# Optimization experiments

Measured on AMD Instinct MI355X. Metric: run time of the kernel, lower is better.

The kernel has to match this reference:

```python
import jax, jax.numpy as jnp
import numpy as np

CUTOFF = 5.0
B, A, N, G, F = 32, 256, 64, 50, 128


def _ssp(v):
    # shifted softplus used by SchNet filter network
    return jax.nn.softplus(v) - jnp.log(2.0).astype(v.dtype)


def setup_inputs() -> dict:
    key = jax.random.key(0)
    ks = jax.random.split(key, 8)
    x = jax.random.normal(ks[0], (B, A, F), dtype=jnp.float32)
    r_ij = jax.random.uniform(ks[1], (B, A, N), dtype=jnp.float32) * 4.5
    f_ij = jax.random.normal(ks[2], (B, A, N, G), dtype=jnp.float32)
    pairwise_mask = jnp.ones((B, A, N), dtype=jnp.float32)
    neighbors = jax.random.randint(ks[3], (B, A, N), 0, A, dtype=jnp.int64)
    in2f_w = jax.random.normal(ks[4], (F, F), dtype=jnp.float32) / np.sqrt(F)
    fw1 = jax.random.normal(ks[5], (G, F), dtype=jnp.float32) / np.sqrt(G)
    fb1 = jnp.zeros((F,), dtype=jnp.float32)
    fw2 = jax.random.normal(ks[6], (F, F), dtype=jnp.float32) / np.sqrt(F)
    fb2 = jnp.zeros((F,), dtype=jnp.float32)
    return {"x": x, "r_ij": r_ij, "f_ij": f_ij, "pairwise_mask": pairwise_mask,
            "neighbors": neighbors, "in2f_w": in2f_w, "fw1": fw1, "fb1": fb1,
            "fw2": fw2, "fb2": fb2}


def reference(x, r_ij, f_ij, pairwise_mask, neighbors, in2f_w, fw1, fb1, fw2, fb2):
    # filter network: Dense(G->F, shifted softplus) -> Dense(F->F, linear)
    W = _ssp(jnp.einsum('bang,gf->banf', f_ij, fw1) + fb1)
    W = jnp.einsum('banh,hf->banf', W, fw2) + fb2          # (B,A,N,F)
    # cosine cutoff
    C = 0.5 * (jnp.cos(r_ij * (jnp.pi / CUTOFF)) + 1.0)
    C = C * (r_ij < CUTOFF).astype(r_ij.dtype)
    W = W * C[..., None]
    # in2f dense (no bias)
    y = jnp.einsum('bai,if->baf', x, in2f_w)               # (B,A,F)
    # gather neighbor features along atom axis
    b_idx = jnp.arange(B)[:, None, None]
    y_nbh = y[b_idx, neighbors]                             # (B,A,N,F)
    # elementwise filter multiply + masked sum over neighbor axis
    out = jnp.sum(y_nbh * W * pairwise_mask[..., None], axis=2)  # (B,A,F)
    return out
```

## Files before the change

### kernel.cpp

```cpp
#include <hip/hip_runtime.h>
#include <hip/hip_bf16.h>
#include <math.h>

#define Bdim 32
#define Adim 256
#define Ndim 64
#define Gdim 50
#define Fdim 128

typedef __attribute__((ext_vector_type(8)))  short short8;
typedef __attribute__((ext_vector_type(16))) float floatx16;

__device__ __forceinline__ unsigned short f2bf_u(float x) {
    __hip_bfloat16 h = __float2bfloat16(x);
    return __builtin_bit_cast(unsigned short, h);
}
__device__ __forceinline__ unsigned pk2bf(float a, float b) {
    return (unsigned)f2bf_u(a) | ((unsigned)f2bf_u(b) << 16);
}
__device__ __forceinline__ float bf2f(unsigned short v) {
    return __builtin_bit_cast(float, ((unsigned)v) << 16);
}
__device__ __forceinline__ float sspf(float v) {
    float t = __expf(-fabsf(v));
    return fmaxf(v, 0.0f) + __logf(1.0f + t) - 0.69314718056f;
}
__device__ __forceinline__ short8 mk8(unsigned a, unsigned b, unsigned c, unsigned d) {
    union { unsigned u[4]; short8 s; } t;
    t.u[0] = a; t.u[1] = b; t.u[2] = c; t.u[3] = d;
    return t.s;
}

__global__ __launch_bounds__(256) void in2f_mfma2(const float* __restrict__ x,
                                                  const float* __restrict__ w,
                                                  unsigned short* __restrict__ y) {
    __shared__ short sWT[128 * 132];
    __shared__ short sX [128 * 132];
    const int tid = threadIdx.x;

#pragma unroll 4
    for (int k = 0; k < 32; ++k) {
        int idx = tid + k * 256;
        float2 v = *(const float2*)(w + 2 * idx);
        int i = idx >> 6;
        int f = (2 * idx) & 127;
        sWT[f * 132 + i]       = (short)f2bf_u(v.x);
        sWT[(f + 1) * 132 + i] = (short)f2bf_u(v.y);
    }
    const float* xb = x + (size_t)blockIdx.x * (128 * 128);
#pragma unroll 4
    for (int k = 0; k < 32; ++k) {
        int idx = tid + k * 256;
        float2 v = *(const float2*)(xb + 2 * idx);
        int row = idx >> 6;
        int i = (2 * idx) & 127;
        *(unsigned*)&sX[row * 132 + i] = pk2bf(v.x, v.y);
    }
    __syncthreads();

    const int wv = tid >> 6, lane = tid & 63, lm = lane & 31, lh = lane >> 5;
    floatx16 acc[4];
#pragma unroll
    for (int jt = 0; jt < 4; ++jt)
#pragma unroll
        for (int e = 0; e < 16; ++e) acc[jt][e] = 0.0f;

#pragma unroll
    for (int ks = 0; ks < 8; ++ks) {
        int g0 = ks * 16 + lh * 8;
        const short* ap = &sX[(wv * 32 + lm) * 132 + g0];
        uint2 a0 = *(const uint2*)ap;
        uint2 a1 = *(const uint2*)(ap + 4);
        short8 a = mk8(a0.x, a0.y, a1.x, a1.y);
#pragma unroll
        for (int jt = 0; jt < 4; ++jt) {
            const short* bp = &sWT[(jt * 32 + lm) * 132 + g0];
            uint2 b0 = *(const uint2*)bp;
            uint2 b1 = *(const uint2*)(bp + 4);
            acc[jt] = __builtin_amdgcn_mfma_f32_32x32x16_bf16(
                a, mk8(b0.x, b0.y, b1.x, b1.y), acc[jt], 0, 0, 0);
        }
    }
    const int rbase = blockIdx.x * 128 + wv * 32;
#pragma unroll
    for (int jt = 0; jt < 4; ++jt)
#pragma unroll
        for (int r = 0; r < 16; ++r) {
            int row = rbase + (r & 3) + 8 * (r >> 2) + 4 * lh;
            y[(size_t)row * 128 + jt * 32 + lm] = f2bf_u(acc[jt][r]);
        }
}

#define SF1 68
#define NSP 4096
#define GRID2 1536

struct FijRegs { float2 p[13]; };

__device__ __forceinline__ FijRegs load_fij(const float* __restrict__ f_ij,
                                            int sp, int row, int lh) {
    FijRegs F;
    const float* base = f_ij + (size_t)sp * (2 * Ndim * Gdim) + row * Gdim;
#pragma unroll
    for (int ks = 0; ks < 3; ++ks) {
        int g0 = 16 * ks + 8 * lh;
#pragma unroll
        for (int j = 0; j < 4; ++j)
            F.p[ks * 4 + j] = *(const float2*)(base + g0 + 2 * j);
    }
    F.p[12] = *(const float2*)(base + 48);
    return F;
}

__device__ __forceinline__ void cf_body(
    int sp, int par, const FijRegs& F, int nsp, FijRegs& Fn,
    const float* __restrict__ f_ij, const float* __restrict__ r_ij,
    const float* __restrict__ mask, const int* __restrict__ nbr,
    const unsigned short* __restrict__ ybf, float* __restrict__ out,
    float4 fb2v, const short* sFw1, const short* sFw2,
    float (*sRed)[2][128], int wv, int lm, int lh, int row)
{
    short8 bfr[4];
#pragma unroll
    for (int ks = 0; ks < 3; ++ks)
        bfr[ks] = mk8(pk2bf(F.p[ks*4+0].x, F.p[ks*4+0].y),
                      pk2bf(F.p[ks*4+1].x, F.p[ks*4+1].y),
                      pk2bf(F.p[ks*4+2].x, F.p[ks*4+2].y),
                      pk2bf(F.p[ks*4+3].x, F.p[ks*4+3].y));
    {
        unsigned u0 = lh ? 0u : pk2bf(F.p[12].x, F.p[12].y);
        unsigned u1 = lh ? 0u : 0x00003F80u;
        bfr[3] = mk8(u0, u1, 0u, 0u);
    }
    if (nsp >= 0) Fn = load_fij(f_ij, nsp, row, lh);

    unsigned A2[8][4];
#pragma unroll
    for (int ft = 0; ft < 4; ++ft) {
        floatx16 a1;
#pragma unroll
        for (int e = 0; e < 16; ++e) a1[e] = 0.0f;
#pragma unroll
        for (int ks = 0; ks < 4; ++ks) {
            const short* ap = &sFw1[(ft * 32 + lm) * SF1 + ks * 16 + lh * 8];
            uint2 a0 = *(const uint2*)ap;
            uint2 a1v = *(const uint2*)(ap + 4);
            a1 = __builtin_amdgcn_mfma_f32_32x32x16_bf16(
                mk8(a0.x, a0.y, a1v.x, a1v.y), bfr[ks], a1, 0, 0, 0);
        }
        unsigned P[8], X[8];
#pragma unroll
        for (int q = 0; q < 8; ++q)
            P[q] = pk2bf(sspf(a1[2 * q]), sspf(a1[2 * q + 1]));
#pragma unroll
        for (int q = 0; q < 8; ++q) X[q] = (unsigned)__shfl_xor((int)P[q], 32);
        A2[2*ft][0]   = lh ? X[2] : P[0];  A2[2*ft][1]   = lh ? X[3] : P[1];
        A2[2*ft][2]   = lh ? P[2] : X[0];  A2[2*ft][3]   = lh ? P[3] : X[1];
        A2[2*ft+1][0] = lh ? X[6] : P[4];  A2[2*ft+1][1] = lh ? X[7] : P[5];
        A2[2*ft+1][2] = lh ? P[6] : X[4];  A2[2*ft+1][3] = lh ? P[7] : X[5];
    }

    floatx16 acc2[4];
#pragma unroll
    for (int jt = 0; jt < 4; ++jt)
#pragma unroll
        for (int e = 0; e < 16; ++e) acc2[jt][e] = 0.0f;
#pragma unroll
    for (int ks = 0; ks < 8; ++ks) {
        short8 a = mk8(A2[ks][0], A2[ks][1], A2[ks][2], A2[ks][3]);
#pragma unroll
        for (int jt = 0; jt < 4; ++jt) {
            int rw = jt * 32 + lm;
            const short* bp = &sFw2[rw * 128 + ((ks * 16 + lh * 8) ^ ((rw & 15) << 3))];
            uint2 b0 = *(const uint2*)bp;
            uint2 b1 = *(const uint2*)(bp + 4);
            acc2[jt] = __builtin_amdgcn_mfma_f32_32x32x16_bf16(
                a, mk8(b0.x, b0.y, b1.x, b1.y), acc2[jt], 0, 0, 0);
        }
    }

    const int site = sp * 2 + (wv >> 1);
    float cmv[16]; int nbv[16];
#pragma unroll
    for (int rq = 0; rq < 4; ++rq) {
        int off = site * Ndim + (wv & 1) * 32 + rq * 8 + lh * 4;
        float4 r4 = *(const float4*)(r_ij + off);
        float4 m4 = *(const float4*)(mask + off);
        int4   n4 = *(const int4*)(nbr + off);
        float rr[4] = { r4.x, r4.y, r4.z, r4.w };
        float mm[4] = { m4.x, m4.y, m4.z, m4.w };
        int   nn[4] = { n4.x, n4.y, n4.z, n4.w };
#pragma unroll
        for (int j = 0; j < 4; ++j) {
            float c = 0.5f * (__cosf(rr[j] * 0.62831853071796f) + 1.0f);
            c = (rr[j] < 5.0f) ? c : 0.0f;
            cmv[rq * 4 + j] = c * mm[j];
            nbv[rq * 4 + j] = nn[j];
        }
    }

    const int bofs = (site >> 8) * Adim;
    float part[4] = {0.f, 0.f, 0.f, 0.f};
#pragma unroll
    for (int r = 0; r < 16; ++r) {
        float cm = cmv[r];
        const unsigned short* yr = ybf + (size_t)(bofs + nbv[r]) * Fdim;
#pragma unroll
        for (int jt = 0; jt < 4; ++jt) {
            float fb2j = (jt == 0) ? fb2v.x : (jt == 1) ? fb2v.y
                       : (jt == 2) ? fb2v.z : fb2v.w;
            float yv = bf2f(yr[jt * 32 + lm]);
            part[jt] += (acc2[jt][r] + fb2j) * cm * yv;
        }
    }
#pragma unroll
    for (int jt = 0; jt < 4; ++jt) part[jt] += __shfl_xor(part[jt], 32);

    const int s = wv >> 1;
    if (wv & 1) {
#pragma unroll
        for (int k = 0; k < 2; ++k)
            sRed[par][s][(2 * lh + k) * 32 + lm] = part[2 * lh + k];
    }
    __syncthreads();
    if (!(wv & 1)) {
#pragma unroll
        for (int k = 0; k < 2; ++k) {
            int jt = 2 * lh + k;
            int f = jt * 32 + lm;
            out[(size_t)site * Fdim + f] = part[jt] + sRed[par][s][f];
        }
    }
}

__global__ __launch_bounds__(256, 3) void cfconv_mfma4(
    const float* __restrict__ r_ij, const float* __restrict__ f_ij,
    const float* __restrict__ mask, const int* __restrict__ nbr,
    const float* __restrict__ fw1, const float* __restrict__ fb1,
    const float* __restrict__ fw2, const float* __restrict__ fb2,
    const unsigned short* __restrict__ ybf, float* __restrict__ out)
{
    __shared__ short sFw1[128 * SF1];
    __shared__ short sFw2[128 * 128];
    __shared__ float sRed[2][2][128];

    const int tid = threadIdx.x, wv = tid >> 6, lane = tid & 63;
    const int lm = lane & 31, lh = lane >> 5;
    const int bid = blockIdx.x;
    const int row = wv * 32 + lm;

    FijRegs FA = load_fij(f_ij, bid, row, lh);

    for (int idx = tid; idx < Gdim * 128; idx += 256) {
        int g = idx >> 7, f = idx & 127;
        sFw1[f * SF1 + g] = (short)f2bf_u(fw1[idx]);
    }
    for (int idx = tid; idx < 128 * 14; idx += 256) {
        int f = idx / 14, g = Gdim + idx % 14;
        sFw1[f * SF1 + g] = (g == Gdim) ? (short)f2bf_u(fb1[f]) : (short)0;
    }
    for (int idx = tid; idx < 128 * 128; idx += 256) {
        int h = idx >> 7, f = idx & 127;
        sFw2[f * 128 + (h ^ ((f & 15) << 3))] = (short)f2bf_u(fw2[idx]);
    }
    float4 fb2v;
    fb2v.x = fb2[lm]; fb2v.y = fb2[32 + lm]; fb2v.z = fb2[64 + lm]; fb2v.w = fb2[96 + lm];
    __syncthreads();

    const int sp1 = bid + GRID2, sp2 = bid + 2 * GRID2;
    FijRegs FB;
    cf_body(bid, 0, FA, sp1, FB, f_ij, r_ij, mask, nbr, ybf, out,
            fb2v, sFw1, sFw2, sRed, wv, lm, lh, row);
    cf_body(sp1, 1, FB, (sp2 < NSP) ? sp2 : -1, FA, f_ij, r_ij, mask, nbr, ybf, out,
            fb2v, sFw1, sFw2, sRed, wv, lm, lh, row);
    if (sp2 < NSP)
        cf_body(sp2, 0, FA, -1, FB, f_ij, r_ij, mask, nbr, ybf, out,
                fb2v, sFw1, sFw2, sRed, wv, lm, lh, row);
}

extern "C" void kernel_launch(void* const* d_in, const int* in_sizes, int n_in,
                              void* d_out, int out_size, void* d_ws, size_t ws_size,
                              hipStream_t stream) {
    const float* x      = (const float*)d_in[0];
    const float* r_ij   = (const float*)d_in[1];
    const float* f_ij   = (const float*)d_in[2];
    const float* mask   = (const float*)d_in[3];
    const int*   nbr    = (const int*)d_in[4];
    const float* in2f_w = (const float*)d_in[5];
    const float* fw1    = (const float*)d_in[6];
    const float* fb1    = (const float*)d_in[7];
    const float* fw2    = (const float*)d_in[8];
    const float* fb2    = (const float*)d_in[9];
    float* out = (float*)d_out;
    unsigned short* y = (unsigned short*)d_ws;

    in2f_mfma2<<<64, 256, 0, stream>>>(x, in2f_w, y);
    cfconv_mfma4<<<GRID2, 256, 0, stream>>>(r_ij, f_ij, mask, nbr,
                                            fw1, fb1, fw2, fb2, y, out);
}
```

Before: 240.7 us.

## Precompute transposed bf16 fw1 in prologue kernel and raise cfconv occupancy

An extra block in the in2f kernel now writes a transposed, bias-augmented bf16 copy of fw1 to workspace. The cfconv kernel reads its first-GEMM A fragments directly from global/L2 instead of staging fw1 in LDS, which shrinks LDS use so launch bounds can rise to 4 blocks per CU with a 2048-block grid doing two sub-problems each. The fw2 LDS layout switches from an XOR swizzle to a padded stride, and the softplus and accumulate steps use log2 and fma forms. In exchange, fw1 fragments now come from global memory on every sub-problem, and the padded layout may cause different LDS bank conflicts.

```diff
diff --git a/kernel.cpp b/kernel.cpp
--- a/kernel.cpp
+++ b/kernel.cpp
@@ -23,7 +23,8 @@
 }
 __device__ __forceinline__ float sspf(float v) {
     float t = __expf(-fabsf(v));
-    return fmaxf(v, 0.0f) + __logf(1.0f + t) - 0.69314718056f;
+    return fmaxf(v, 0.0f) +
+           fmaf(__log2f(1.0f + t), 0.69314718056f, -0.69314718056f);
 }
 __device__ __forceinline__ short8 mk8(unsigned a, unsigned b, unsigned c, unsigned d) {
     union { unsigned u[4]; short8 s; } t;
@@ -33,10 +34,21 @@
 
 __global__ __launch_bounds__(256) void in2f_mfma2(const float* __restrict__ x,
                                                   const float* __restrict__ w,
-                                                  unsigned short* __restrict__ y) {
+                                                  unsigned short* __restrict__ y,
+                                                  const float* __restrict__ fw1,
+                                                  const float* __restrict__ fb1,
+                                                  unsigned short* __restrict__ fw1t) {
+    const int tid = threadIdx.x;
+    if (blockIdx.x == 64) {
+        for (int idx = tid; idx < 128 * 64; idx += 256) {
+            int f = idx >> 6, g = idx & 63;
+            float v = (g < Gdim) ? fw1[g * 128 + f] : ((g == Gdim) ? fb1[f] : 0.0f);
+            fw1t[idx] = f2bf_u(v);
+        }
+        return;
+    }
     __shared__ short sWT[128 * 132];
     __shared__ short sX [128 * 132];
-    const int tid = threadIdx.x;
 
 #pragma unroll 4
     for (int k = 0; k < 32; ++k) {
@@ -91,9 +103,9 @@
         }
 }
 
-#define SF1 68
+#define SF2 132
 #define NSP 4096
-#define GRID2 1536
+#define GRID2 2048
 
 struct FijRegs { float2 p[13]; };
 
@@ -116,8 +128,9 @@
     int sp, int par, const FijRegs& F, int nsp, FijRegs& Fn,
     const float* __restrict__ f_ij, const float* __restrict__ r_ij,
     const float* __restrict__ mask, const int* __restrict__ nbr,
+    const unsigned short* __restrict__ fw1t,
     const unsigned short* __restrict__ ybf, float* __restrict__ out,
-    float4 fb2v, const short* sFw1, const short* sFw2,
+    float4 fb2v, const short* sFw2,
     float (*sRed)[2][128], int wv, int lm, int lh, int row)
 {
     short8 bfr[4];
@@ -140,13 +153,11 @@
         floatx16 a1;
 #pragma unroll
         for (int e = 0; e < 16; ++e) a1[e] = 0.0f;
+        const unsigned short* fwp = fw1t + ((ft * 32 + lm) * 64 + lh * 8);
 #pragma unroll
         for (int ks = 0; ks < 4; ++ks) {
-            const short* ap = &sFw1[(ft * 32 + lm) * SF1 + ks * 16 + lh * 8];
-            uint2 a0 = *(const uint2*)ap;
-            uint2 a1v = *(const uint2*)(ap + 4);
-            a1 = __builtin_amdgcn_mfma_f32_32x32x16_bf16(
-                mk8(a0.x, a0.y, a1v.x, a1v.y), bfr[ks], a1, 0, 0, 0);
+            short8 a = *(const short8*)(fwp + ks * 16);
+            a1 = __builtin_amdgcn_mfma_f32_32x32x16_bf16(a, bfr[ks], a1, 0, 0, 0);
         }
         unsigned P[8], X[8];
 #pragma unroll
@@ -170,8 +181,7 @@
         short8 a = mk8(A2[ks][0], A2[ks][1], A2[ks][2], A2[ks][3]);
 #pragma unroll
         for (int jt = 0; jt < 4; ++jt) {
-            int rw = jt * 32 + lm;
-            const short* bp = &sFw2[rw * 128 + ((ks * 16 + lh * 8) ^ ((rw & 15) << 3))];
+            const short* bp = &sFw2[(jt * 32 + lm) * SF2 + ks * 16 + lh * 8];
             uint2 b0 = *(const uint2*)bp;
             uint2 b1 = *(const uint2*)(bp + 4);
             acc2[jt] = __builtin_amdgcn_mfma_f32_32x32x16_bf16(
@@ -209,8 +219,8 @@
         for (int jt = 0; jt < 4; ++jt) {
             float fb2j = (jt == 0) ? fb2v.x : (jt == 1) ? fb2v.y
                        : (jt == 2) ? fb2v.z : fb2v.w;
-            float yv = bf2f(yr[jt * 32 + lm]);
-            part[jt] += (acc2[jt][r] + fb2j) * cm * yv;
+            float t = (acc2[jt][r] + fb2j) * cm;
+            part[jt] = fmaf(t, bf2f(yr[jt * 32 + lm]), part[jt]);
         }
     }
 #pragma unroll
@@ -233,15 +243,14 @@
     }
 }
 
-__global__ __launch_bounds__(256, 3) void cfconv_mfma4(
+__global__ __launch_bounds__(256, 4) void cfconv_mfma5(
     const float* __restrict__ r_ij, const float* __restrict__ f_ij,
     const float* __restrict__ mask, const int* __restrict__ nbr,
-    const float* __restrict__ fw1, const float* __restrict__ fb1,
-    const float* __restrict__ fw2, const float* __restrict__ fb2,
+    const unsigned short* __restrict__ fw1t, const float* __restrict__ fw2,
+    const float* __restrict__ fb2,
     const unsigned short* __restrict__ ybf, float* __restrict__ out)
 {
-    __shared__ short sFw1[128 * SF1];
-    __shared__ short sFw2[128 * 128];
+    __shared__ short sFw2[128 * SF2];
     __shared__ float sRed[2][2][128];
 
     const int tid = threadIdx.x, wv = tid >> 6, lane = tid & 63;
@@ -251,31 +260,20 @@
 
     FijRegs FA = load_fij(f_ij, bid, row, lh);
 
-    for (int idx = tid; idx < Gdim * 128; idx += 256) {
-        int g = idx >> 7, f = idx & 127;
-        sFw1[f * SF1 + g] = (short)f2bf_u(fw1[idx]);
-    }
-    for (int idx = tid; idx < 128 * 14; idx += 256) {
-        int f = idx / 14, g = Gdim + idx % 14;
-        sFw1[f * SF1 + g] = (g == Gdim) ? (short)f2bf_u(fb1[f]) : (short)0;
-    }
     for (int idx = tid; idx < 128 * 128; idx += 256) {
         int h = idx >> 7, f = idx & 127;
-        sFw2[f * 128 + (h ^ ((f & 15) << 3))] = (short)f2bf_u(fw2[idx]);
+        sFw2[f * SF2 + h] = (short)f2bf_u(fw2[idx]);
     }
     float4 fb2v;
     fb2v.x = fb2[lm]; fb2v.y = fb2[32 + lm]; fb2v.z = fb2[64 + lm]; fb2v.w = fb2[96 + lm];
     __syncthreads();
 
-    const int sp1 = bid + GRID2, sp2 = bid + 2 * GRID2;
+    const int sp1 = bid + GRID2;
     FijRegs FB;
-    cf_body(bid, 0, FA, sp1, FB, f_ij, r_ij, mask, nbr, ybf, out,
-            fb2v, sFw1, sFw2, sRed, wv, lm, lh, row);
-    cf_body(sp1, 1, FB, (sp2 < NSP) ? sp2 : -1, FA, f_ij, r_ij, mask, nbr, ybf, out,
-            fb2v, sFw1, sFw2, sRed, wv, lm, lh, row);
-    if (sp2 < NSP)
-        cf_body(sp2, 0, FA, -1, FB, f_ij, r_ij, mask, nbr, ybf, out,
-                fb2v, sFw1, sFw2, sRed, wv, lm, lh, row);
+    cf_body(bid, 0, FA, sp1, FB, f_ij, r_ij, mask, nbr, fw1t, ybf, out,
+            fb2v, sFw2, sRed, wv, lm, lh, row);
+    cf_body(sp1, 1, FB, -1, FA, f_ij, r_ij, mask, nbr, fw1t, ybf, out,
+            fb2v, sFw2, sRed, wv, lm, lh, row);
 }
 
 extern "C" void kernel_launch(void* const* d_in, const int* in_sizes, int n_in,
@@ -292,9 +290,10 @@
     const float* fw2    = (const float*)d_in[8];
     const float* fb2    = (const float*)d_in[9];
     float* out = (float*)d_out;
-    unsigned short* y = (unsigned short*)d_ws;
-
-    in2f_mfma2<<<64, 256, 0, stream>>>(x, in2f_w, y);
-    cfconv_mfma4<<<GRID2, 256, 0, stream>>>(r_ij, f_ij, mask, nbr,
-                                            fw1, fb1, fw2, fb2, y, out);
-}
+    unsigned short* y    = (unsigned short*)d_ws;
+    unsigned short* fw1t = (unsigned short*)((char*)d_ws + (size_t)(Bdim*Adim*Fdim)*2);
+
+    in2f_mfma2<<<65, 256, 0, stream>>>(x, in2f_w, y, fw1, fb1, fw1t);
+    cfconv_mfma5<<<GRID2, 256, 0, stream>>>(r_ij, f_ij, mask, nbr,
+                                            fw1t, fw2, fb2, y, out);
+}
```

After: 268.1 us. +11.4%, slower.
